# Kernel tuning notes

Hardware: AMD Instinct MI355X
Metric: run time of the kernel (lower is better)

## Reference

```python
import jax, jax.numpy as jnp
import numpy as np

N = 4096
IN = 64          # input_size
QD = 16          # query_vector_dim
CI = 2 * IN + 1  # 129, MLP_Param input dim


def _xavier(key, shape):
    fan_in, fan_out = shape[-2], shape[-1]
    bound = float(np.sqrt(6.0 / (fan_in + fan_out)))
    return jax.random.uniform(key, shape, jnp.float32, -bound, bound)


def setup_inputs() -> dict:
    key = jax.random.key(0)
    ks = jax.random.split(key, 10)
    return {
        "x": jax.random.normal(ks[0], (N, IN + 1), jnp.float32),
        "h": jax.random.normal(ks[1], (N, IN), jnp.float32),
        "query_vectors": jax.random.normal(ks[2], (N, QD), jnp.float32),
        "adj": jax.random.uniform(ks[3], (N, N), jnp.float32),
        "nodes_ind": jnp.arange(N, dtype=jnp.int64 if jax.config.jax_enable_x64 else jnp.int32),
        "W_r": _xavier(ks[4], (QD, CI, IN)),
        "b_r": _xavier(ks[5], (QD, IN)),
        "W_u": _xavier(ks[6], (QD, CI, IN)),
        "b_u": _xavier(ks[7], (QD, IN)),
        "W_c": _xavier(ks[8], (QD, CI, IN)),
        "b_c": _xavier(ks[9], (QD, IN)),
    }


def _mlp_param(xv, q, W, b):
    # per-node dynamic weights: [n, CI, IN]
    Wn = jnp.einsum('nd,dio->nio', q, W)
    return jnp.einsum('ni,nio->no', xv, Wn) + q @ b


def reference(x, h, query_vectors, adj, nodes_ind, W_r, b_r, W_u, b_u, W_c, b_c):
    combined = adj @ jnp.concatenate([x, h], axis=-1)          # [N, 129]
    cg = combined[nodes_ind]                                    # [M, 129]
    r = jax.nn.sigmoid(_mlp_param(cg, query_vectors, W_r, b_r))
    u = jax.nn.sigmoid(_mlp_param(cg, query_vectors, W_u, b_u))
    h2 = h.at[nodes_ind].set(r * h[nodes_ind])                  # h[nodes_ind] = r*h[nodes_ind]
    combined_new = jnp.concatenate([x, h2], axis=-1)[nodes_ind]  # no adj mixing second time
    cand = jnp.tanh(_mlp_param(combined_new, query_vectors, W_c, b_c))
    return (1.0 - u) * h2[nodes_ind] + u * cand
```

## Files before the change

kernel.cpp:

```cpp
#include <hip/hip_runtime.h>
#include <math.h>


#define NN   4096
#define XCC  65
#define HCC  64
#define QDIM 16
#define CI   129
#define CST  132
#define AKST 520
#define XVST 148
#define GSTRIDE 147456

typedef unsigned short u16;
typedef __attribute__((ext_vector_type(4))) unsigned short ushort4_t;
typedef __attribute__((ext_vector_type(8))) unsigned short ushort8_t;
typedef __attribute__((ext_vector_type(8))) short bf16x8;
typedef __attribute__((ext_vector_type(16))) float f32x16;

__device__ __forceinline__ void split2(float a, u16& hi, u16& lo) {
  unsigned u = __float_as_uint(a);
  hi = (u16)(u >> 16);
  float rec = __uint_as_float(u & 0xFFFF0000u);
  float lf = a - rec;
  unsigned v = __float_as_uint(lf);
  v += 0x7FFF + ((v >> 16) & 1);
  lo = (u16)(v >> 16);
}

__device__ __forceinline__ void gload_lds16(const void* gsrc, void* ldst) {
  __builtin_amdgcn_global_load_lds(
      (const __attribute__((address_space(1))) unsigned int*)gsrc,
      (__attribute__((address_space(3))) unsigned int*)ldst, 16, 0, 0);
}

__global__ __launch_bounds__(256) void k0_pack(const float* __restrict__ x,
                                               const float* __restrict__ h,
                                               u16* __restrict__ Bh,
                                               u16* __restrict__ Bl,
                                               const float* __restrict__ Wr,
                                               const float* __restrict__ Wu,
                                               const float* __restrict__ Wc,
                                               u16* __restrict__ Wh,
                                               u16* __restrict__ Wl) {
  __shared__ float sT[64][161];
  const int t = threadIdx.x;
  if (blockIdx.x < 64) {
    const int n0 = blockIdx.x * 64;
    for (int f = t; f < 64 * XCC; f += 256) {
      int n = f / XCC, c = f - n * XCC;
      sT[n][c] = x[(size_t)(n0 + n) * XCC + c];
    }
    for (int f = t; f < 64 * HCC; f += 256) {
      int n = f >> 6, c = f & 63;
      sT[n][XCC + c] = h[(size_t)(n0 + n) * HCC + c];
    }
    for (int f = t; f < 64 * 31; f += 256) {
      int n = f / 31, c = f - n * 31;
      sT[n][CI + c] = 0.f;
    }
    __syncthreads();
    for (int idx = t; idx < 5 * 4 * 64; idx += 256) {
      const int lane = idx & 63;
      const int ksl = (idx >> 6) & 3;
      const int ct = idx >> 8;
      const int nl = ksl * 16 + (lane >> 5) * 8;
      const int feat = ct * 32 + (lane & 31);
      ushort8_t vh, vl;
#pragma unroll
      for (int j = 0; j < 8; ++j) {
        u16 hi, lo; split2(sT[nl + j][feat], hi, lo);
        vh[j] = hi; vl[j] = lo;
      }
      const size_t off = (((size_t)ct * 256 + (blockIdx.x * 4) + ksl) * 64 + lane) * 8;
      *(ushort8_t*)(Bh + off) = vh;
      *(ushort8_t*)(Bl + off) = vl;
    }
  } else {
    int gid = (blockIdx.x - 64) * 256 + t;
    if (gid >= 3 * 16 * 2 * 9 * 64) return;
    int lane = gid & 63;
    int rest = gid >> 6;
    int kst = rest % 9; rest /= 9;
    int ct = rest & 1; rest >>= 1;
    int d = rest & 15; rest >>= 4;
    const float* W = (rest == 0) ? Wr : (rest == 1 ? Wu : Wc);
    const int o = ct * 32 + (lane & 31);
    const int i0 = kst * 16 + (lane >> 5) * 8;
    ushort8_t vh, vl;
#pragma unroll
    for (int j = 0; j < 8; ++j) {
      int i = i0 + j;
      float v = (i < CI) ? W[((size_t)d * CI + i) * 64 + o] : 0.f;
      u16 hi, lo; split2(v, hi, lo);
      vh[j] = hi; vl[j] = lo;
    }
    const size_t off = (size_t)gid * 8;
    *(ushort8_t*)(Wh + off) = vh;
    *(ushort8_t*)(Wl + off) = vl;
  }
}

template <int SPK>
__global__ __launch_bounds__(256, 4) void k1_mfma(const float* __restrict__ adj,
                                                  const u16* __restrict__ Bh,
                                                  const u16* __restrict__ Bl,
                                                  float* __restrict__ P1) {
  constexpr int KLEN = 4096 / SPK;
  constexpr int STEPS = KLEN / 16;
  __shared__ u16 sAh[2][2][64][8];
  __shared__ u16 sAl[2][2][64][8];
  __shared__ u16 sB[3][10][512];
  __shared__ u16 sScratch[512];
  const int t = threadIdx.x;
  const int lane = t & 63;
  const int w = t >> 6;
  const int rgrp = w & 1;
  const int cthalf = w >> 1;
  const int m0 = blockIdx.x * 64;
  const int sp = blockIdx.y;
  const int ct0 = cthalf ? 3 : 0;
  const int R = t >> 2;
  const int ksts = t & 3;
  const int srg = R >> 5, srl = R & 31;
  const int skh = ksts >> 1, sj0 = (ksts & 1) * 4;

  f32x16 a0, a1, a2;
#pragma unroll
  for (int r = 0; r < 16; ++r) { a0[r] = 0.f; a1[r] = 0.f; a2[r] = 0.f; }

  const float* aptr = adj + (size_t)(m0 + R) * NN + sp * KLEN + ksts * 4;
  float4 va, vb, vc;

#define LOADA(it, tgt) tgt = *(const float4*)(aptr + (it) * 16);

#define CONV4(src, abuf)                                                       \
  {                                                                            \
    u16 h0, h1, h2, h3, l0, l1, l2, l3;                                        \
    split2(src.x, h0, l0); split2(src.y, h1, l1);                              \
    split2(src.z, h2, l2); split2(src.w, h3, l3);                              \
    ushort4_t hv = {h0, h1, h2, h3};                                           \
    ushort4_t lv = {l0, l1, l2, l3};                                           \
    *(ushort4_t*)&sAh[abuf][srg][srl + 32 * skh][sj0] = hv;                    \
    *(ushort4_t*)&sAl[abuf][srg][srl + 32 * skh][sj0] = lv;                    \
  }

#define BDMA(it, bbuf)                                                         \
  {                                                                            \
    _Pragma("unroll")                                                          \
    for (int j = 0; j < 3; ++j) {                                              \
      const int c = w + 4 * j;                                                 \
      const int ct = (c < 10) ? (c >> 1) : 0;                                  \
      const int hl = (c < 10) ? (c & 1) : 0;                                   \
      const int ks = sp * STEPS + (it);                                        \
      const u16* src =                                                         \
          (hl ? Bl : Bh) + (((size_t)ct * 256 + ks) * 64 + lane) * 8;          \
      gload_lds16(src, (c < 10) ? &sB[bbuf][c][0] : &sScratch[0]);             \
    }                                                                          \
  }

#define BAR(N)                                                                 \
  asm volatile("s_waitcnt vmcnt(" #N ") lgkmcnt(0)" ::: "memory");             \
  __builtin_amdgcn_sched_barrier(0);                                           \
  __builtin_amdgcn_s_barrier();                                                \
  __builtin_amdgcn_sched_barrier(0);

#define COMPUTE(abuf, bbuf)                                                    \
  {                                                                            \
    bf16x8 ah = *(const bf16x8*)&sAh[abuf][rgrp][lane][0];                     \
    bf16x8 al = *(const bf16x8*)&sAl[abuf][rgrp][lane][0];                     \
    const int cb = ct0 * 2;                                                    \
    bf16x8 b0h = *(const bf16x8*)&sB[bbuf][cb + 0][lane * 8];                  \
    bf16x8 b0l = *(const bf16x8*)&sB[bbuf][cb + 1][lane * 8];                  \
    bf16x8 b1h = *(const bf16x8*)&sB[bbuf][cb + 2][lane * 8];                  \
    bf16x8 b1l = *(const bf16x8*)&sB[bbuf][cb + 3][lane * 8];                  \
    a0 = __builtin_amdgcn_mfma_f32_32x32x16_bf16(ah, b0h, a0, 0, 0, 0);        \
    a1 = __builtin_amdgcn_mfma_f32_32x32x16_bf16(ah, b1h, a1, 0, 0, 0);        \
    a0 = __builtin_amdgcn_mfma_f32_32x32x16_bf16(al, b0h, a0, 0, 0, 0);        \
    a1 = __builtin_amdgcn_mfma_f32_32x32x16_bf16(al, b1h, a1, 0, 0, 0);        \
    a0 = __builtin_amdgcn_mfma_f32_32x32x16_bf16(ah, b0l, a0, 0, 0, 0);        \
    a1 = __builtin_amdgcn_mfma_f32_32x32x16_bf16(ah, b1l, a1, 0, 0, 0);        \
    if (cthalf == 0) {                                                         \
      bf16x8 b2h = *(const bf16x8*)&sB[bbuf][cb + 4][lane * 8];                \
      bf16x8 b2l = *(const bf16x8*)&sB[bbuf][cb + 5][lane * 8];                \
      a2 = __builtin_amdgcn_mfma_f32_32x32x16_bf16(ah, b2h, a2, 0, 0, 0);      \
      a2 = __builtin_amdgcn_mfma_f32_32x32x16_bf16(al, b2h, a2, 0, 0, 0);      \
      a2 = __builtin_amdgcn_mfma_f32_32x32x16_bf16(ah, b2l, a2, 0, 0, 0);      \
    }                                                                          \
  }

  LOADA(0, va);
  BDMA(0, 0);
  LOADA(1, vb);
  BDMA(1, 1);
  LOADA(2, vc);
  CONV4(va, 0);
  BAR(5)
#pragma unroll
  for (int it = 0; it < STEPS; ++it) {
    const int abuf = it & 1;
    const int bbuf = it % 3;
    if (it < STEPS - 2) BDMA(it + 2, (it + 2) % 3);
    if (it <= STEPS - 4) {
      if ((it % 3) == 0) { LOADA(it + 3, va); }
      else if ((it % 3) == 1) { LOADA(it + 3, vb); }
      else { LOADA(it + 3, vc); }
    }
    COMPUTE(abuf, bbuf);
    if (it < STEPS - 1) {
      if (((it + 1) % 3) == 0) { CONV4(va, abuf ^ 1); }
      else if (((it + 1) % 3) == 1) { CONV4(vb, abuf ^ 1); }
      else { CONV4(vc, abuf ^ 1); }
    }
    if (it <= STEPS - 4) { BAR(5) }
    else if (it == STEPS - 3) { BAR(4) }
    else if (it == STEPS - 2) { BAR(0) }
  }
#undef LOADA
#undef CONV4
#undef BDMA
#undef BAR
#undef COMPUTE
  float* outp = P1 + (size_t)sp * NN * CST;
  const int colb = lane & 31;
  const int rbase = m0 + rgrp * 32 + 4 * (lane >> 5);
  {
    const int colg = ct0 * 32 + colb;
#pragma unroll
    for (int r = 0; r < 16; ++r)
      outp[(size_t)(rbase + (r & 3) + 8 * (r >> 2)) * CST + colg] = a0[r];
  }
  {
    const int colg = (ct0 + 1) * 32 + colb;
    if (colg < CST) {
#pragma unroll
      for (int r = 0; r < 16; ++r)
        outp[(size_t)(rbase + (r & 3) + 8 * (r >> 2)) * CST + colg] = a1[r];
    }
  }
  if (cthalf == 0) {
    const int colg = 64 + colb;
#pragma unroll
    for (int r = 0; r < 16; ++r)
      outp[(size_t)(rbase + (r & 3) + 8 * (r >> 2)) * CST + colg] = a2[r];
  }
}


#define PACKA()                                                                \
  for (int s = t; s < 9 * 64; s += 512) {                                      \
    int kst = s >> 6, l = s & 63;                                              \
    int row = l & 31, k0i = kst * 16 + (l >> 5) * 8;                           \
    ushort8_t vh, vl;                                                          \
    _Pragma("unroll")                                                          \
    for (int j = 0; j < 8; ++j) {                                              \
      u16 hi, lo; split2(sXV[row][k0i + j], hi, lo);                           \
      vh[j] = hi; vl[j] = lo;                                                  \
    }                                                                          \
    *(ushort8_t*)&sAh[kst * AKST + l * 8] = vh;                                \
    *(ushort8_t*)&sAl[kst * AKST + l * 8] = vl;                                \
  }

template <int SPK>
__global__ __launch_bounds__(512) void k23_fused(
    const float* __restrict__ P1, const float* __restrict__ x,
    const float* __restrict__ h, const float* __restrict__ q,
    const u16* __restrict__ Wh, const u16* __restrict__ Wl,
    const float* __restrict__ br, const float* __restrict__ bu,
    const float* __restrict__ bc, float* __restrict__ out) {
  __shared__ float sXV[32][XVST];
  __shared__ u16 sAh[9 * AKST], sAl[9 * AKST];
  __shared__ float sQ[32][16];
  __shared__ float sX0[8][16][64];
  __shared__ float sX1[8][16][64];
  __shared__ float sX2[8][16][64];
  const int t = threadIdx.x;
  const int n0 = blockIdx.x * 32;
  const int cto = blockIdx.y;
  for (int f = t; f < 32 * 33; f += 512) {
    int n = f / 33, c4 = f - n * 33;
    const float* p = P1 + (size_t)(n0 + n) * CST + c4 * 4;
    float sx = 0.f, sy = 0.f, sz = 0.f, sw = 0.f;
#pragma unroll
    for (int sp = 0; sp < SPK; ++sp) {
      float4 v = *(const float4*)(p + (size_t)sp * NN * CST);
      sx += v.x; sy += v.y; sz += v.z; sw += v.w;
    }
    sXV[n][c4 * 4 + 0] = sx; sXV[n][c4 * 4 + 1] = sy;
    sXV[n][c4 * 4 + 2] = sz; sXV[n][c4 * 4 + 3] = sw;
  }
  for (int f = t; f < 32 * 3; f += 512) {
    float4 z = {0, 0, 0, 0};
    *(float4*)&sXV[f / 3][132 + (f % 3) * 4] = z;
  }
  sQ[t >> 4][t & 15] = q[(size_t)(n0 + (t >> 4)) * QDIM + (t & 15)];
  __syncthreads();
  PACKA();
  __syncthreads();
  for (int f = t; f < 32 * 65; f += 512) {
    int n = f / 65, i = f - n * 65;
    sXV[n][i] = x[(size_t)(n0 + n) * XCC + i];
  }
  const int lane = t & 63, dh = t >> 6;

  f32x16 aR0, aR1, aU;
#pragma unroll
  for (int r = 0; r < 16; ++r) { aR0[r] = 0.f; aR1[r] = 0.f; aU[r] = 0.f; }
#pragma unroll
  for (int dd = 0; dd < 2; ++dd) {
    const int d = dh * 2 + dd;
    const size_t bR0 = (((size_t)d * 2 + 0) * 9 * 64 + lane) * 8;
    const size_t bR1 = (((size_t)d * 2 + 1) * 9 * 64 + lane) * 8;
    const size_t bU  = (((size_t)d * 2 + cto) * 9 * 64 + lane) * 8 + GSTRIDE;
    f32x16 t0, t1, t2;
#pragma unroll
    for (int r = 0; r < 16; ++r) { t0[r] = 0.f; t1[r] = 0.f; t2[r] = 0.f; }
#pragma unroll
    for (int kst = 0; kst < 9; ++kst) {
      bf16x8 ah = *(const bf16x8*)&sAh[kst * AKST + lane * 8];
      bf16x8 al = *(const bf16x8*)&sAl[kst * AKST + lane * 8];
      bf16x8 b0h = *(const bf16x8*)(Wh + bR0 + kst * 512);
      bf16x8 b0l = *(const bf16x8*)(Wl + bR0 + kst * 512);
      bf16x8 b1h = *(const bf16x8*)(Wh + bR1 + kst * 512);
      bf16x8 b1l = *(const bf16x8*)(Wl + bR1 + kst * 512);
      bf16x8 buh = *(const bf16x8*)(Wh + bU + kst * 512);
      bf16x8 bul = *(const bf16x8*)(Wl + bU + kst * 512);
      t0 = __builtin_amdgcn_mfma_f32_32x32x16_bf16(ah, b0h, t0, 0, 0, 0);
      t1 = __builtin_amdgcn_mfma_f32_32x32x16_bf16(ah, b1h, t1, 0, 0, 0);
      t2 = __builtin_amdgcn_mfma_f32_32x32x16_bf16(ah, buh, t2, 0, 0, 0);
      t0 = __builtin_amdgcn_mfma_f32_32x32x16_bf16(al, b0h, t0, 0, 0, 0);
      t1 = __builtin_amdgcn_mfma_f32_32x32x16_bf16(al, b1h, t1, 0, 0, 0);
      t2 = __builtin_amdgcn_mfma_f32_32x32x16_bf16(al, buh, t2, 0, 0, 0);
      t0 = __builtin_amdgcn_mfma_f32_32x32x16_bf16(ah, b0l, t0, 0, 0, 0);
      t1 = __builtin_amdgcn_mfma_f32_32x32x16_bf16(ah, b1l, t1, 0, 0, 0);
      t2 = __builtin_amdgcn_mfma_f32_32x32x16_bf16(ah, bul, t2, 0, 0, 0);
    }
#pragma unroll
    for (int r = 0; r < 16; ++r) {
      int node = (r & 3) + 8 * (r >> 2) + 4 * (lane >> 5);
      float qd = sQ[node][d];
      aR0[r] += qd * t0[r]; aR1[r] += qd * t1[r]; aU[r] += qd * t2[r];
    }
  }
#pragma unroll
  for (int r = 0; r < 16; ++r) {
    sX0[dh][r][lane] = aR0[r];
    sX1[dh][r][lane] = aR1[r];
    sX2[dh][r][lane] = aU[r];
  }
  __syncthreads();

  auto add_bias = [&](const float* bias, int node, int col, float pre) {
#pragma unroll
    for (int d = 0; d < 16; ++d) pre += sQ[node][d] * bias[(size_t)d * 64 + col];
    return pre;
  };

  float r0p[2], r1p[2], up[2];
#pragma unroll
  for (int i = 0; i < 2; ++i) {
    const int rr = dh * 2 + i;
    float a = 0.f, b = 0.f, c = 0.f;
#pragma unroll
    for (int wv = 0; wv < 8; ++wv) {
      a += sX0[wv][rr][lane];
      b += sX1[wv][rr][lane];
      c += sX2[wv][rr][lane];
    }
    r0p[i] = a; r1p[i] = b; up[i] = c;
  }

  const int col0 = lane & 31, col1 = 32 + col0, colu = cto * 32 + col0;
  float uval[2], h2own[2];
#pragma unroll
  for (int i = 0; i < 2; ++i) {
    const int rr = dh * 2 + i;
    const int node = (rr & 3) + 8 * (rr >> 2) + 4 * (lane >> 5);
    float pr0 = add_bias(br, node, col0, r0p[i]);
    float pr1 = add_bias(br, node, col1, r1p[i]);
    float pu  = add_bias(bu, node, colu, up[i]);
    float rg0 = 1.f / (1.f + expf(-pr0));
    float rg1 = 1.f / (1.f + expf(-pr1));
    uval[i] = 1.f / (1.f + expf(-pu));
    float h2a = rg0 * h[(size_t)(n0 + node) * HCC + col0];
    float h2b = rg1 * h[(size_t)(n0 + node) * HCC + col1];
    sXV[node][XCC + col0] = h2a;
    sXV[node][XCC + col1] = h2b;
    h2own[i] = cto ? h2b : h2a;
  }
  __syncthreads();
  PACKA();
  __syncthreads();

  {
    const u16* gh = Wh + (size_t)2 * GSTRIDE;
    const u16* gl = Wl + (size_t)2 * GSTRIDE;
    f32x16 acc;
#pragma unroll
    for (int r = 0; r < 16; ++r) acc[r] = 0.f;
#pragma unroll
    for (int dd = 0; dd < 2; ++dd) {
      const int d = dh * 2 + dd;
      const size_t bb = (((size_t)d * 2 + cto) * 9 * 64 + lane) * 8;
      f32x16 t0, t1, t2;
#pragma unroll
      for (int r = 0; r < 16; ++r) { t0[r] = 0.f; t1[r] = 0.f; t2[r] = 0.f; }
#pragma unroll
      for (int kst = 0; kst < 9; ++kst) {
        bf16x8 ah = *(const bf16x8*)&sAh[kst * AKST + lane * 8];
        bf16x8 al = *(const bf16x8*)&sAl[kst * AKST + lane * 8];
        bf16x8 bh = *(const bf16x8*)(gh + bb + kst * 512);
        bf16x8 bl = *(const bf16x8*)(gl + bb + kst * 512);
        t0 = __builtin_amdgcn_mfma_f32_32x32x16_bf16(ah, bh, t0, 0, 0, 0);
        t1 = __builtin_amdgcn_mfma_f32_32x32x16_bf16(al, bh, t1, 0, 0, 0);
        t2 = __builtin_amdgcn_mfma_f32_32x32x16_bf16(ah, bl, t2, 0, 0, 0);
      }
#pragma unroll
      for (int r = 0; r < 16; ++r) {
        int node = (r & 3) + 8 * (r >> 2) + 4 * (lane >> 5);
        acc[r] += sQ[node][d] * (t0[r] + t1[r] + t2[r]);
      }
    }
#pragma unroll
    for (int r = 0; r < 16; ++r) sX0[dh][r][lane] = acc[r];
  }
  __syncthreads();
#pragma unroll
  for (int i = 0; i < 2; ++i) {
    const int rr = dh * 2 + i;
    const int node = (rr & 3) + 8 * (rr >> 2) + 4 * (lane >> 5);
    float s = 0.f;
#pragma unroll
    for (int wv = 0; wv < 8; ++wv) s += sX0[wv][rr][lane];
    float pc = add_bias(bc, node, colu, s);
    float cand = tanhf(pc);
    out[(size_t)(n0 + node) * HCC + colu] =
        (1.f - uval[i]) * h2own[i] + uval[i] * cand;
  }
}

extern "C" void kernel_launch(void* const* d_in, const int* in_sizes, int n_in,
                              void* d_out, int out_size, void* d_ws, size_t ws_size,
                              hipStream_t stream) {
  const float* x   = (const float*)d_in[0];
  const float* h   = (const float*)d_in[1];
  const float* q   = (const float*)d_in[2];
  const float* adj = (const float*)d_in[3];
  const float* Wr  = (const float*)d_in[5];
  const float* br  = (const float*)d_in[6];
  const float* Wu  = (const float*)d_in[7];
  const float* bu  = (const float*)d_in[8];
  const float* Wc  = (const float*)d_in[9];
  const float* bc  = (const float*)d_in[10];
  float* out = (float*)d_out;

  const size_t NEED16 = (size_t)16 * NN * CST * 4 + 2162688 + 10485760 + 1769472;
  const int spk = (ws_size >= NEED16) ? 16 : 8;

  char* ws = (char*)d_ws;
  const size_t OFF_P1 = 0;
  const size_t OFF_XV = OFF_P1 + (size_t)spk * NN * CST * 4;
  const size_t OFF_BP = OFF_XV + (size_t)NN * CST * 4;
  const size_t OFF_WH = OFF_BP + (size_t)2 * 5 * 256 * 64 * 8 * 2;
  const size_t OFF_WL = OFF_WH + (size_t)3 * GSTRIDE * 2;
  float* P1 = (float*)(ws + OFF_P1);
  u16*   Bh = (u16*)(ws + OFF_BP);
  u16*   Bl = (u16*)(ws + OFF_BP + (size_t)5 * 256 * 64 * 8 * 2);
  u16*   Wh = (u16*)(ws + OFF_WH);
  u16*   Wl = (u16*)(ws + OFF_WL);

  hipLaunchKernelGGL(k0_pack, dim3(280), dim3(256), 0, stream,
                     x, h, Bh, Bl, Wr, Wu, Wc, Wh, Wl);
  if (spk == 16) {
    hipLaunchKernelGGL(k1_mfma<16>, dim3(64, 16), dim3(256), 0, stream, adj, Bh, Bl, P1);
    hipLaunchKernelGGL(k23_fused<16>, dim3(128, 2), dim3(512), 0, stream,
                       P1, x, h, q, Wh, Wl, br, bu, bc, out);
  } else {
    hipLaunchKernelGGL(k1_mfma<8>, dim3(64, 8), dim3(256), 0, stream, adj, Bh, Bl, P1);
    hipLaunchKernelGGL(k23_fused<8>, dim3(128, 2), dim3(512), 0, stream,
                       P1, x, h, q, Wh, Wl, br, bu, bc, out);
  }
}
```

Baseline: 64.43 us.

## Split fused gate/candidate kernel into separate gate and candidate kernels

```diff
diff --git a/kernel.cpp b/kernel.cpp
--- a/kernel.cpp
+++ b/kernel.cpp
@@ -11,6 +11,7 @@
 #define AKST 520
 #define XVST 148
 #define GSTRIDE 147456
+#define SPK  8
 
 typedef unsigned short u16;
 typedef __attribute__((ext_vector_type(4))) unsigned short ushort4_t;
@@ -101,12 +102,12 @@
   }
 }
 
-template <int SPK>
+template <int SPKT>
 __global__ __launch_bounds__(256, 4) void k1_mfma(const float* __restrict__ adj,
                                                   const u16* __restrict__ Bh,
                                                   const u16* __restrict__ Bl,
                                                   float* __restrict__ P1) {
-  constexpr int KLEN = 4096 / SPK;
+  constexpr int KLEN = 4096 / SPKT;
   constexpr int STEPS = KLEN / 16;
   __shared__ u16 sAh[2][2][64][8];
   __shared__ u16 sAl[2][2][64][8];
@@ -246,7 +247,6 @@
   }
 }
 
-
 #define PACKA()                                                                \
   for (int s = t; s < 9 * 64; s += 512) {                                      \
     int kst = s >> 6, l = s & 63;                                              \
@@ -261,22 +261,20 @@
     *(ushort8_t*)&sAl[kst * AKST + l * 8] = vl;                                \
   }
 
-template <int SPK>
-__global__ __launch_bounds__(512) void k23_fused(
-    const float* __restrict__ P1, const float* __restrict__ x,
-    const float* __restrict__ h, const float* __restrict__ q,
-    const u16* __restrict__ Wh, const u16* __restrict__ Wl,
-    const float* __restrict__ br, const float* __restrict__ bu,
-    const float* __restrict__ bc, float* __restrict__ out) {
+__global__ __launch_bounds__(512, 2) void k2_gate(
+    const float* __restrict__ P1, const float* __restrict__ h,
+    const float* __restrict__ q, const u16* __restrict__ Wh,
+    const u16* __restrict__ Wl, const float* __restrict__ br,
+    const float* __restrict__ bu, float* __restrict__ U,
+    float* __restrict__ H2) {
   __shared__ float sXV[32][XVST];
   __shared__ u16 sAh[9 * AKST], sAl[9 * AKST];
   __shared__ float sQ[32][16];
   __shared__ float sX0[8][16][64];
   __shared__ float sX1[8][16][64];
-  __shared__ float sX2[8][16][64];
   const int t = threadIdx.x;
   const int n0 = blockIdx.x * 32;
-  const int cto = blockIdx.y;
+  const int g = blockIdx.y;
   for (int f = t; f < 32 * 33; f += 512) {
     int n = f / 33, c4 = f - n * 33;
     const float* p = P1 + (size_t)(n0 + n) * CST + c4 * 4;
@@ -297,134 +295,141 @@
   __syncthreads();
   PACKA();
   __syncthreads();
-  for (int f = t; f < 32 * 65; f += 512) {
-    int n = f / 65, i = f - n * 65;
-    sXV[n][i] = x[(size_t)(n0 + n) * XCC + i];
-  }
   const int lane = t & 63, dh = t >> 6;
-
-  f32x16 aR0, aR1, aU;
-#pragma unroll
-  for (int r = 0; r < 16; ++r) { aR0[r] = 0.f; aR1[r] = 0.f; aU[r] = 0.f; }
+  const u16* gh = Wh + (size_t)g * GSTRIDE;
+  const u16* gl = Wl + (size_t)g * GSTRIDE;
+
+  f32x16 aC0, aC1;
+#pragma unroll
+  for (int r = 0; r < 16; ++r) { aC0[r] = 0.f; aC1[r] = 0.f; }
 #pragma unroll
   for (int dd = 0; dd < 2; ++dd) {
     const int d = dh * 2 + dd;
-    const size_t bR0 = (((size_t)d * 2 + 0) * 9 * 64 + lane) * 8;
-    const size_t bR1 = (((size_t)d * 2 + 1) * 9 * 64 + lane) * 8;
-    const size_t bU  = (((size_t)d * 2 + cto) * 9 * 64 + lane) * 8 + GSTRIDE;
-    f32x16 t0, t1, t2;
-#pragma unroll
-    for (int r = 0; r < 16; ++r) { t0[r] = 0.f; t1[r] = 0.f; t2[r] = 0.f; }
+    const size_t b0 = (((size_t)d * 2 + 0) * 576 + lane) * 8;
+    const size_t b1 = (((size_t)d * 2 + 1) * 576 + lane) * 8;
+    f32x16 t00, t01, t02, t10, t11, t12;
+#pragma unroll
+    for (int r = 0; r < 16; ++r) {
+      t00[r] = 0.f; t01[r] = 0.f; t02[r] = 0.f;
+      t10[r] = 0.f; t11[r] = 0.f; t12[r] = 0.f;
+    }
 #pragma unroll
     for (int kst = 0; kst < 9; ++kst) {
       bf16x8 ah = *(const bf16x8*)&sAh[kst * AKST + lane * 8];
       bf16x8 al = *(const bf16x8*)&sAl[kst * AKST + lane * 8];
-      bf16x8 b0h = *(const bf16x8*)(Wh + bR0 + kst * 512);
-      bf16x8 b0l = *(const bf16x8*)(Wl + bR0 + kst * 512);
-      bf16x8 b1h = *(const bf16x8*)(Wh + bR1 + kst * 512);
-      bf16x8 b1l = *(const bf16x8*)(Wl + bR1 + kst * 512);
-      bf16x8 buh = *(const bf16x8*)(Wh + bU + kst * 512);
-      bf16x8 bul = *(const bf16x8*)(Wl + bU + kst * 512);
-      t0 = __builtin_amdgcn_mfma_f32_32x32x16_bf16(ah, b0h, t0, 0, 0, 0);
-      t1 = __builtin_amdgcn_mfma_f32_32x32x16_bf16(ah, b1h, t1, 0, 0, 0);
-      t2 = __builtin_amdgcn_mfma_f32_32x32x16_bf16(ah, buh, t2, 0, 0, 0);
-      t0 = __builtin_amdgcn_mfma_f32_32x32x16_bf16(al, b0h, t0, 0, 0, 0);
-      t1 = __builtin_amdgcn_mfma_f32_32x32x16_bf16(al, b1h, t1, 0, 0, 0);
-      t2 = __builtin_amdgcn_mfma_f32_32x32x16_bf16(al, buh, t2, 0, 0, 0);
-      t0 = __builtin_amdgcn_mfma_f32_32x32x16_bf16(ah, b0l, t0, 0, 0, 0);
-      t1 = __builtin_amdgcn_mfma_f32_32x32x16_bf16(ah, b1l, t1, 0, 0, 0);
-      t2 = __builtin_amdgcn_mfma_f32_32x32x16_bf16(ah, bul, t2, 0, 0, 0);
+      bf16x8 b0h = *(const bf16x8*)(gh + b0 + kst * 512);
+      bf16x8 b0l = *(const bf16x8*)(gl + b0 + kst * 512);
+      bf16x8 b1h = *(const bf16x8*)(gh + b1 + kst * 512);
+      bf16x8 b1l = *(const bf16x8*)(gl + b1 + kst * 512);
+      t00 = __builtin_amdgcn_mfma_f32_32x32x16_bf16(ah, b0h, t00, 0, 0, 0);
+      t10 = __builtin_amdgcn_mfma_f32_32x32x16_bf16(ah, b1h, t10, 0, 0, 0);
+      t01 = __builtin_amdgcn_mfma_f32_32x32x16_bf16(al, b0h, t01, 0, 0, 0);
+      t11 = __builtin_amdgcn_mfma_f32_32x32x16_bf16(al, b1h, t11, 0, 0, 0);
+      t02 = __builtin_amdgcn_mfma_f32_32x32x16_bf16(ah, b0l, t02, 0, 0, 0);
+      t12 = __builtin_amdgcn_mfma_f32_32x32x16_bf16(ah, b1l, t12, 0, 0, 0);
     }
 #pragma unroll
     for (int r = 0; r < 16; ++r) {
       int node = (r & 3) + 8 * (r >> 2) + 4 * (lane >> 5);
       float qd = sQ[node][d];
-      aR0[r] += qd * t0[r]; aR1[r] += qd * t1[r]; aU[r] += qd * t2[r];
+      aC0[r] += qd * (t00[r] + t01[r] + t02[r]);
+      aC1[r] += qd * (t10[r] + t11[r] + t12[r]);
     }
   }
 #pragma unroll
   for (int r = 0; r < 16; ++r) {
-    sX0[dh][r][lane] = aR0[r];
-    sX1[dh][r][lane] = aR1[r];
-    sX2[dh][r][lane] = aU[r];
-  }
-  __syncthreads();
-
-  auto add_bias = [&](const float* bias, int node, int col, float pre) {
-#pragma unroll
-    for (int d = 0; d < 16; ++d) pre += sQ[node][d] * bias[(size_t)d * 64 + col];
-    return pre;
-  };
-
-  float r0p[2], r1p[2], up[2];
-#pragma unroll
-  for (int i = 0; i < 2; ++i) {
-    const int rr = dh * 2 + i;
-    float a = 0.f, b = 0.f, c = 0.f;
-#pragma unroll
-    for (int wv = 0; wv < 8; ++wv) {
-      a += sX0[wv][rr][lane];
-      b += sX1[wv][rr][lane];
-      c += sX2[wv][rr][lane];
-    }
-    r0p[i] = a; r1p[i] = b; up[i] = c;
-  }
-
-  const int col0 = lane & 31, col1 = 32 + col0, colu = cto * 32 + col0;
-  float uval[2], h2own[2];
+    sX0[dh][r][lane] = aC0[r];
+    sX1[dh][r][lane] = aC1[r];
+  }
+  __syncthreads();
+  const float* bias = g ? bu : br;
+  const int col0 = lane & 31, col1 = 32 + col0;
 #pragma unroll
   for (int i = 0; i < 2; ++i) {
     const int rr = dh * 2 + i;
     const int node = (rr & 3) + 8 * (rr >> 2) + 4 * (lane >> 5);
-    float pr0 = add_bias(br, node, col0, r0p[i]);
-    float pr1 = add_bias(br, node, col1, r1p[i]);
-    float pu  = add_bias(bu, node, colu, up[i]);
-    float rg0 = 1.f / (1.f + expf(-pr0));
-    float rg1 = 1.f / (1.f + expf(-pr1));
-    uval[i] = 1.f / (1.f + expf(-pu));
-    float h2a = rg0 * h[(size_t)(n0 + node) * HCC + col0];
-    float h2b = rg1 * h[(size_t)(n0 + node) * HCC + col1];
-    sXV[node][XCC + col0] = h2a;
-    sXV[node][XCC + col1] = h2b;
-    h2own[i] = cto ? h2b : h2a;
-  }
+    float s0 = 0.f, s1 = 0.f;
+#pragma unroll
+    for (int wv = 0; wv < 8; ++wv) {
+      s0 += sX0[wv][rr][lane];
+      s1 += sX1[wv][rr][lane];
+    }
+#pragma unroll
+    for (int d = 0; d < 16; ++d) {
+      float qd = sQ[node][d];
+      s0 += qd * bias[(size_t)d * 64 + col0];
+      s1 += qd * bias[(size_t)d * 64 + col1];
+    }
+    float sg0 = 1.f / (1.f + expf(-s0));
+    float sg1 = 1.f / (1.f + expf(-s1));
+    const int g0 = (n0 + node) * 64 + col0;
+    const int g1 = (n0 + node) * 64 + col1;
+    if (g == 0) {
+      H2[g0] = sg0 * h[g0];
+      H2[g1] = sg1 * h[g1];
+    } else {
+      U[g0] = sg0;
+      U[g1] = sg1;
+    }
+  }
+}
+
+__global__ __launch_bounds__(512, 2) void k3_cand(
+    const float* __restrict__ x, const float* __restrict__ H2,
+    const float* __restrict__ q, const u16* __restrict__ Wh,
+    const u16* __restrict__ Wl, const float* __restrict__ bc,
+    const float* __restrict__ U, float* __restrict__ out) {
+  __shared__ float sXV[32][XVST];
+  __shared__ u16 sAh[9 * AKST], sAl[9 * AKST];
+  __shared__ float sQ[32][16];
+  __shared__ float sX0[8][16][64];
+  const int t = threadIdx.x;
+  const int n0 = blockIdx.x * 32;
+  const int cto = blockIdx.y;
+  for (int f = t; f < 32 * 144; f += 512) {
+    int n = f / 144, i = f - n * 144;
+    float v = 0.f;
+    if (i < XCC) v = x[(size_t)(n0 + n) * XCC + i];
+    else if (i < CI) v = H2[(size_t)(n0 + n) * HCC + (i - XCC)];
+    sXV[n][i] = v;
+  }
+  sQ[t >> 4][t & 15] = q[(size_t)(n0 + (t >> 4)) * QDIM + (t & 15)];
   __syncthreads();
   PACKA();
   __syncthreads();
-
-  {
-    const u16* gh = Wh + (size_t)2 * GSTRIDE;
-    const u16* gl = Wl + (size_t)2 * GSTRIDE;
-    f32x16 acc;
-#pragma unroll
-    for (int r = 0; r < 16; ++r) acc[r] = 0.f;
-#pragma unroll
-    for (int dd = 0; dd < 2; ++dd) {
-      const int d = dh * 2 + dd;
-      const size_t bb = (((size_t)d * 2 + cto) * 9 * 64 + lane) * 8;
-      f32x16 t0, t1, t2;
-#pragma unroll
-      for (int r = 0; r < 16; ++r) { t0[r] = 0.f; t1[r] = 0.f; t2[r] = 0.f; }
-#pragma unroll
-      for (int kst = 0; kst < 9; ++kst) {
-        bf16x8 ah = *(const bf16x8*)&sAh[kst * AKST + lane * 8];
-        bf16x8 al = *(const bf16x8*)&sAl[kst * AKST + lane * 8];
-        bf16x8 bh = *(const bf16x8*)(gh + bb + kst * 512);
-        bf16x8 bl = *(const bf16x8*)(gl + bb + kst * 512);
-        t0 = __builtin_amdgcn_mfma_f32_32x32x16_bf16(ah, bh, t0, 0, 0, 0);
-        t1 = __builtin_amdgcn_mfma_f32_32x32x16_bf16(al, bh, t1, 0, 0, 0);
-        t2 = __builtin_amdgcn_mfma_f32_32x32x16_bf16(ah, bl, t2, 0, 0, 0);
-      }
-#pragma unroll
-      for (int r = 0; r < 16; ++r) {
-        int node = (r & 3) + 8 * (r >> 2) + 4 * (lane >> 5);
-        acc[r] += sQ[node][d] * (t0[r] + t1[r] + t2[r]);
-      }
-    }
-#pragma unroll
-    for (int r = 0; r < 16; ++r) sX0[dh][r][lane] = acc[r];
-  }
-  __syncthreads();
+  const int lane = t & 63, dh = t >> 6;
+  const u16* gh = Wh + (size_t)2 * GSTRIDE;
+  const u16* gl = Wl + (size_t)2 * GSTRIDE;
+  f32x16 acc;
+#pragma unroll
+  for (int r = 0; r < 16; ++r) acc[r] = 0.f;
+#pragma unroll
+  for (int dd = 0; dd < 2; ++dd) {
+    const int d = dh * 2 + dd;
+    const size_t bb = (((size_t)d * 2 + cto) * 576 + lane) * 8;
+    f32x16 t0, t1, t2;
+#pragma unroll
+    for (int r = 0; r < 16; ++r) { t0[r] = 0.f; t1[r] = 0.f; t2[r] = 0.f; }
+#pragma unroll
+    for (int kst = 0; kst < 9; ++kst) {
+      bf16x8 ah = *(const bf16x8*)&sAh[kst * AKST + lane * 8];
+      bf16x8 al = *(const bf16x8*)&sAl[kst * AKST + lane * 8];
+      bf16x8 bh = *(const bf16x8*)(gh + bb + kst * 512);
+      bf16x8 bl = *(const bf16x8*)(gl + bb + kst * 512);
+      t0 = __builtin_amdgcn_mfma_f32_32x32x16_bf16(ah, bh, t0, 0, 0, 0);
+      t1 = __builtin_amdgcn_mfma_f32_32x32x16_bf16(al, bh, t1, 0, 0, 0);
+      t2 = __builtin_amdgcn_mfma_f32_32x32x16_bf16(ah, bl, t2, 0, 0, 0);
+    }
+#pragma unroll
+    for (int r = 0; r < 16; ++r) {
+      int node = (r & 3) + 8 * (r >> 2) + 4 * (lane >> 5);
+      acc[r] += sQ[node][d] * (t0[r] + t1[r] + t2[r]);
+    }
+  }
+#pragma unroll
+  for (int r = 0; r < 16; ++r) sX0[dh][r][lane] = acc[r];
+  __syncthreads();
+  const int colu = cto * 32 + (lane & 31);
 #pragma unroll
   for (int i = 0; i < 2; ++i) {
     const int rr = dh * 2 + i;
@@ -432,10 +437,12 @@
     float s = 0.f;
 #pragma unroll
     for (int wv = 0; wv < 8; ++wv) s += sX0[wv][rr][lane];
-    float pc = add_bias(bc, node, colu, s);
-    float cand = tanhf(pc);
-    out[(size_t)(n0 + node) * HCC + colu] =
-        (1.f - uval[i]) * h2own[i] + uval[i] * cand;
+#pragma unroll
+    for (int d = 0; d < 16; ++d) s += sQ[node][d] * bc[(size_t)d * 64 + colu];
+    float cand = tanhf(s);
+    const int gidx = (n0 + node) * 64 + colu;
+    float u = U[gidx], h2 = H2[gidx];
+    out[gidx] = (1.f - u) * h2 + u * cand;
   }
 }
 
@@ -454,30 +461,27 @@
   const float* bc  = (const float*)d_in[10];
   float* out = (float*)d_out;
 
-  const size_t NEED16 = (size_t)16 * NN * CST * 4 + 2162688 + 10485760 + 1769472;
-  const int spk = (ws_size >= NEED16) ? 16 : 8;
-
   char* ws = (char*)d_ws;
   const size_t OFF_P1 = 0;
-  const size_t OFF_XV = OFF_P1 + (size_t)spk * NN * CST * 4;
-  const size_t OFF_BP = OFF_XV + (size_t)NN * CST * 4;
+  const size_t OFF_BP = OFF_P1 + (size_t)SPK * NN * CST * 4;
   const size_t OFF_WH = OFF_BP + (size_t)2 * 5 * 256 * 64 * 8 * 2;
   const size_t OFF_WL = OFF_WH + (size_t)3 * GSTRIDE * 2;
+  const size_t OFF_U  = OFF_WL + (size_t)3 * GSTRIDE * 2;
+  const size_t OFF_H2 = OFF_U + (size_t)NN * HCC * 4;
   float* P1 = (float*)(ws + OFF_P1);
   u16*   Bh = (u16*)(ws + OFF_BP);
   u16*   Bl = (u16*)(ws + OFF_BP + (size_t)5 * 256 * 64 * 8 * 2);
   u16*   Wh = (u16*)(ws + OFF_WH);
   u16*   Wl = (u16*)(ws + OFF_WL);
+  float* U  = (float*)(ws + OFF_U);
+  float* H2 = (float*)(ws + OFF_H2);
 
   hipLaunchKernelGGL(k0_pack, dim3(280), dim3(256), 0, stream,
                      x, h, Bh, Bl, Wr, Wu, Wc, Wh, Wl);
-  if (spk == 16) {
-    hipLaunchKernelGGL(k1_mfma<16>, dim3(64, 16), dim3(256), 0, stream, adj, Bh, Bl, P1);
-    hipLaunchKernelGGL(k23_fused<16>, dim3(128, 2), dim3(512), 0, stream,
-                       P1, x, h, q, Wh, Wl, br, bu, bc, out);
-  } else {
-    hipLaunchKernelGGL(k1_mfma<8>, dim3(64, 8), dim3(256), 0, stream, adj, Bh, Bl, P1);
-    hipLaunchKernelGGL(k23_fused<8>, dim3(128, 2), dim3(512), 0, stream,
-                       P1, x, h, q, Wh, Wl, br, bu, bc, out);
-  }
-}
+  hipLaunchKernelGGL(k1_mfma<SPK>, dim3(64, SPK), dim3(256), 0, stream,
+                     adj, Bh, Bl, P1);
+  hipLaunchKernelGGL(k2_gate, dim3(128, 2), dim3(512), 0, stream,
+                     P1, h, q, Wh, Wl, br, bu, U, H2);
+  hipLaunchKernelGGL(k3_cand, dim3(128, 2), dim3(512), 0, stream,
+                     x, H2, q, Wh, Wl, bc, U, out);
+}
```

Measured after the change: 72.52 us. 12.6% more time.

## Replace split-K partial buffers with float atomic accumulation into XV

Applied to the files above, without the earlier changes.

```diff
diff --git a/kernel.cpp b/kernel.cpp
--- a/kernel.cpp
+++ b/kernel.cpp
@@ -42,11 +42,17 @@
                                                const float* __restrict__ Wu,
                                                const float* __restrict__ Wc,
                                                u16* __restrict__ Wh,
-                                               u16* __restrict__ Wl) {
+                                               u16* __restrict__ Wl,
+                                               float* __restrict__ XV) {
   __shared__ float sT[64][161];
   const int t = threadIdx.x;
   if (blockIdx.x < 64) {
     const int n0 = blockIdx.x * 64;
+    for (int f = t; f < 64 * 33; f += 256) {
+      int n = f / 33, c4 = f - n * 33;
+      float4 z = {0, 0, 0, 0};
+      *(float4*)(XV + (size_t)(n0 + n) * CST + c4 * 4) = z;
+    }
     for (int f = t; f < 64 * XCC; f += 256) {
       int n = f / XCC, c = f - n * XCC;
       sT[n][c] = x[(size_t)(n0 + n) * XCC + c];
@@ -101,12 +107,11 @@
   }
 }
 
-template <int SPK>
 __global__ __launch_bounds__(256, 4) void k1_mfma(const float* __restrict__ adj,
                                                   const u16* __restrict__ Bh,
                                                   const u16* __restrict__ Bl,
-                                                  float* __restrict__ P1) {
-  constexpr int KLEN = 4096 / SPK;
+                                                  float* __restrict__ XV) {
+  constexpr int KLEN = 256;
   constexpr int STEPS = KLEN / 16;
   __shared__ u16 sAh[2][2][64][8];
   __shared__ u16 sAl[2][2][64][8];
@@ -221,31 +226,29 @@
 #undef BDMA
 #undef BAR
 #undef COMPUTE
-  float* outp = P1 + (size_t)sp * NN * CST;
   const int colb = lane & 31;
   const int rbase = m0 + rgrp * 32 + 4 * (lane >> 5);
   {
     const int colg = ct0 * 32 + colb;
 #pragma unroll
     for (int r = 0; r < 16; ++r)
-      outp[(size_t)(rbase + (r & 3) + 8 * (r >> 2)) * CST + colg] = a0[r];
+      unsafeAtomicAdd(&XV[(size_t)(rbase + (r & 3) + 8 * (r >> 2)) * CST + colg], a0[r]);
   }
   {
     const int colg = (ct0 + 1) * 32 + colb;
     if (colg < CST) {
 #pragma unroll
       for (int r = 0; r < 16; ++r)
-        outp[(size_t)(rbase + (r & 3) + 8 * (r >> 2)) * CST + colg] = a1[r];
+        unsafeAtomicAdd(&XV[(size_t)(rbase + (r & 3) + 8 * (r >> 2)) * CST + colg], a1[r]);
     }
   }
   if (cthalf == 0) {
     const int colg = 64 + colb;
 #pragma unroll
     for (int r = 0; r < 16; ++r)
-      outp[(size_t)(rbase + (r & 3) + 8 * (r >> 2)) * CST + colg] = a2[r];
-  }
-}
-
+      unsafeAtomicAdd(&XV[(size_t)(rbase + (r & 3) + 8 * (r >> 2)) * CST + colg], a2[r]);
+  }
+}
 
 #define PACKA()                                                                \
   for (int s = t; s < 9 * 64; s += 512) {                                      \
@@ -261,9 +264,8 @@
     *(ushort8_t*)&sAl[kst * AKST + l * 8] = vl;                                \
   }
 
-template <int SPK>
 __global__ __launch_bounds__(512) void k23_fused(
-    const float* __restrict__ P1, const float* __restrict__ x,
+    const float* __restrict__ XV, const float* __restrict__ x,
     const float* __restrict__ h, const float* __restrict__ q,
     const u16* __restrict__ Wh, const u16* __restrict__ Wl,
     const float* __restrict__ br, const float* __restrict__ bu,
@@ -279,15 +281,8 @@
   const int cto = blockIdx.y;
   for (int f = t; f < 32 * 33; f += 512) {
     int n = f / 33, c4 = f - n * 33;
-    const float* p = P1 + (size_t)(n0 + n) * CST + c4 * 4;
-    float sx = 0.f, sy = 0.f, sz = 0.f, sw = 0.f;
-#pragma unroll
-    for (int sp = 0; sp < SPK; ++sp) {
-      float4 v = *(const float4*)(p + (size_t)sp * NN * CST);
-      sx += v.x; sy += v.y; sz += v.z; sw += v.w;
-    }
-    sXV[n][c4 * 4 + 0] = sx; sXV[n][c4 * 4 + 1] = sy;
-    sXV[n][c4 * 4 + 2] = sz; sXV[n][c4 * 4 + 3] = sw;
+    float4 v = *(const float4*)(XV + (size_t)(n0 + n) * CST + c4 * 4);
+    *(float4*)&sXV[n][c4 * 4] = v;
   }
   for (int f = t; f < 32 * 3; f += 512) {
     float4 z = {0, 0, 0, 0};
@@ -309,9 +304,9 @@
 #pragma unroll
   for (int dd = 0; dd < 2; ++dd) {
     const int d = dh * 2 + dd;
-    const size_t bR0 = (((size_t)d * 2 + 0) * 9 * 64 + lane) * 8;
-    const size_t bR1 = (((size_t)d * 2 + 1) * 9 * 64 + lane) * 8;
-    const size_t bU  = (((size_t)d * 2 + cto) * 9 * 64 + lane) * 8 + GSTRIDE;
+    const size_t bR0 = (((size_t)d * 2 + 0) * 576 + lane) * 8;
+    const size_t bR1 = (((size_t)d * 2 + 1) * 576 + lane) * 8;
+    const size_t bU  = (((size_t)d * 2 + cto) * 576 + lane) * 8 + GSTRIDE;
     f32x16 t0, t1, t2;
 #pragma unroll
     for (int r = 0; r < 16; ++r) { t0[r] = 0.f; t1[r] = 0.f; t2[r] = 0.f; }
@@ -401,7 +396,7 @@
 #pragma unroll
     for (int dd = 0; dd < 2; ++dd) {
       const int d = dh * 2 + dd;
-      const size_t bb = (((size_t)d * 2 + cto) * 9 * 64 + lane) * 8;
+      const size_t bb = (((size_t)d * 2 + cto) * 576 + lane) * 8;
       f32x16 t0, t1, t2;
 #pragma unroll
       for (int r = 0; r < 16; ++r) { t0[r] = 0.f; t1[r] = 0.f; t2[r] = 0.f; }
@@ -432,8 +427,8 @@
     float s = 0.f;
 #pragma unroll
     for (int wv = 0; wv < 8; ++wv) s += sX0[wv][rr][lane];
-    float pc = add_bias(bc, node, colu, s);
-    float cand = tanhf(pc);
+    float pc2 = add_bias(bc, node, colu, s);
+    float cand = tanhf(pc2);
     out[(size_t)(n0 + node) * HCC + colu] =
         (1.f - uval[i]) * h2own[i] + uval[i] * cand;
   }
@@ -454,30 +449,21 @@
   const float* bc  = (const float*)d_in[10];
   float* out = (float*)d_out;
 
-  const size_t NEED16 = (size_t)16 * NN * CST * 4 + 2162688 + 10485760 + 1769472;
-  const int spk = (ws_size >= NEED16) ? 16 : 8;
-
   char* ws = (char*)d_ws;
-  const size_t OFF_P1 = 0;
-  const size_t OFF_XV = OFF_P1 + (size_t)spk * NN * CST * 4;
+  const size_t OFF_XV = 0;
   const size_t OFF_BP = OFF_XV + (size_t)NN * CST * 4;
   const size_t OFF_WH = OFF_BP + (size_t)2 * 5 * 256 * 64 * 8 * 2;
   const size_t OFF_WL = OFF_WH + (size_t)3 * GSTRIDE * 2;
-  float* P1 = (float*)(ws + OFF_P1);
+  float* XV = (float*)(ws + OFF_XV);
   u16*   Bh = (u16*)(ws + OFF_BP);
   u16*   Bl = (u16*)(ws + OFF_BP + (size_t)5 * 256 * 64 * 8 * 2);
   u16*   Wh = (u16*)(ws + OFF_WH);
   u16*   Wl = (u16*)(ws + OFF_WL);
 
   hipLaunchKernelGGL(k0_pack, dim3(280), dim3(256), 0, stream,
-                     x, h, Bh, Bl, Wr, Wu, Wc, Wh, Wl);
-  if (spk == 16) {
-    hipLaunchKernelGGL(k1_mfma<16>, dim3(64, 16), dim3(256), 0, stream, adj, Bh, Bl, P1);
-    hipLaunchKernelGGL(k23_fused<16>, dim3(128, 2), dim3(512), 0, stream,
-                       P1, x, h, q, Wh, Wl, br, bu, bc, out);
-  } else {
-    hipLaunchKernelGGL(k1_mfma<8>, dim3(64, 8), dim3(256), 0, stream, adj, Bh, Bl, P1);
-    hipLaunchKernelGGL(k23_fused<8>, dim3(128, 2), dim3(512), 0, stream,
-                       P1, x, h, q, Wh, Wl, br, bu, bc, out);
-  }
-}
+                     x, h, Bh, Bl, Wr, Wu, Wc, Wh, Wl, XV);
+  hipLaunchKernelGGL(k1_mfma, dim3(64, 16), dim3(256), 0, stream,
+                     adj, Bh, Bl, XV);
+  hipLaunchKernelGGL(k23_fused, dim3(128, 2), dim3(512), 0, stream,
+                     XV, x, h, q, Wh, Wl, br, bu, bc, out);
+}
```

Result: slower. 90.17 us (+40.0%).
